# Kernel tuning notes

Measured on AMD Instinct MI355X. Metric: run time of the kernel, lower is better.

## Reference

```python
import jax, jax.numpy as jnp
import numpy as np

B, L, E, H = 32, 2048, 512, 512


def setup_inputs() -> dict:
    key = jax.random.key(0)
    k1, k2, k3, k4 = jax.random.split(key, 4)
    encodings = jax.random.normal(k1, (B, L, E), dtype=jnp.float32)
    lengths = jax.random.randint(k2, (B,), 1, L + 1, dtype=jnp.int32)
    # Glorot-ish scaled params
    W_h = jax.random.normal(k3, (E, H), dtype=jnp.float32) / np.sqrt(E)
    b_h = jnp.zeros((H,), dtype=jnp.float32)
    W_c = jax.random.normal(k4, (H, E), dtype=jnp.float32) / np.sqrt(H)
    return {"encodings": encodings, "lengths": lengths, "W_h": W_h, "b_h": b_h, "W_c": W_c}


def reference(encodings, lengths, W_h, b_h, W_c):
    # encodings: [B, L, E] padded ragged pack; lengths: [B] valid lengths
    mask = jnp.arange(encodings.shape[1])[None, :] < lengths[:, None]  # [B, L]
    # hidden_layer with tanh nonlinearity (TimeDistributedLinear)
    h = jnp.tanh(jnp.einsum('ble,eh->blh', encodings, W_h) + b_h)  # [B, L, H]
    # context_vector (no bias) -> per-feature attention logits [B, L, E]
    att = jnp.einsum('blh,he->ble', h, W_c)
    # timedistributed_softmax: softmax over time axis per sample, per feature
    att = jnp.where(mask[:, :, None], att, -jnp.inf)
    att = jax.nn.softmax(att, axis=1)  # padded positions get weight 0
    # weighted sum over time -> [B, E], then unsqueeze(1)
    out = jnp.sum(att * encodings, axis=1)[:, None, :]  # [B, 1, E]
    return out
```

## Files before the change

### kernel.cpp

```cpp
#include <hip/hip_runtime.h>
#include <math.h>

#define BB 32
#define LL 2048
#define EE 512
#define HH 512
#define WSL 32

typedef __bf16 bf16_t;
typedef bf16_t bf16x8 __attribute__((ext_vector_type(8)));
typedef float f32x4 __attribute__((ext_vector_type(4)));
typedef unsigned short u16x8 __attribute__((ext_vector_type(8)));

__device__ __forceinline__ unsigned short f2bf(float f) {
  unsigned int u = __builtin_bit_cast(unsigned int, f);
  unsigned int r = (u + 0x7FFFu + ((u >> 16) & 1u)) >> 16;
  return (unsigned short)r;
}
__device__ __forceinline__ float bf2f(unsigned short s) {
  unsigned int u = ((unsigned int)s) << 16;
  return __builtin_bit_cast(float, u);
}
__device__ __forceinline__ bf16x8 ld_frag(const unsigned short* p) {
  u16x8 raw = *(const u16x8*)p;
  return __builtin_bit_cast(bf16x8, raw);
}
__device__ __forceinline__ float tanh_fast(float x) {
  x = fminf(fmaxf(x, -15.f), 15.f);
  float e2 = __expf(2.f * x);
  return (e2 - 1.f) / (e2 + 1.f);
}

__device__ __forceinline__ void w_issue(const unsigned short* __restrict__ Wt,
                                        int rbase, int k0, int lane, u16x8 t[4]) {
  const unsigned short* g = Wt + (size_t)(rbase + (lane >> 2)) * 512 + k0 + (lane & 3) * 8;
#pragma unroll
  for (int i = 0; i < 4; i++) t[i] = *(const u16x8*)(g + i * 16 * 512);
}
__device__ __forceinline__ void w_write(unsigned short* buf, int lane, const u16x8 t[4]) {
  unsigned short* d = buf + (lane >> 2) * WSL + (lane & 3) * 8;
#pragma unroll
  for (int i = 0; i < 4; i++) *(u16x8*)(d + i * 16 * WSL) = t[i];
}

__global__ __launch_bounds__(256) void prep_w(
    const float* __restrict__ Wh, const float* __restrict__ Wc,
    unsigned short* __restrict__ WhT, unsigned short* __restrict__ WcT,
    int* __restrict__ q)
{
  if (blockIdx.x == 0 && blockIdx.y == 0 && threadIdx.x == 0) *q = 0;
  const float* src = blockIdx.y ? Wc : Wh;
  unsigned short* dst = blockIdx.y ? WcT : WhT;
  const int tr = (blockIdx.x >> 3) * 64;
  const int tc = (blockIdx.x & 7) * 64;
  const int tid = threadIdx.x;
  __shared__ float tile[64][65];
  for (int i = tid; i < 64 * 16; i += 256) {
    const int r = i >> 4, c4 = (i & 15) << 2;
    const float4 v = *(const float4*)(src + (size_t)(tr + r) * 512 + tc + c4);
    tile[r][c4 + 0] = v.x; tile[r][c4 + 1] = v.y;
    tile[r][c4 + 2] = v.z; tile[r][c4 + 3] = v.w;
  }
  __syncthreads();
  for (int i = tid; i < 64 * 16; i += 256) {
    const int r = i >> 4, c4 = (i & 15) << 2;
    ushort4 pk;
    pk.x = f2bf(tile[c4 + 0][r]); pk.y = f2bf(tile[c4 + 1][r]);
    pk.z = f2bf(tile[c4 + 2][r]); pk.w = f2bf(tile[c4 + 3][r]);
    *(ushort4*)(dst + (size_t)(tc + r) * 512 + tr + c4) = pk;
  }
}

__global__ __launch_bounds__(512, 2) void attn_main(
    const float* __restrict__ enc, const int* __restrict__ lens,
    const unsigned short* __restrict__ WhT, const float* __restrict__ bh,
    const unsigned short* __restrict__ WcT,
    float* __restrict__ pm, float* __restrict__ ps, float* __restrict__ po,
    int* __restrict__ q, int C, int Lc)
{
  const int tid  = threadIdx.x;
  const int wave = tid >> 6;
  const int lane = tid & 63;
  const int quad = lane >> 4;
  const int l15  = lane & 15;
  const int wbase = wave * 64;

  __shared__ __align__(16) unsigned short ebuf[2][32 * 520];
  __shared__ __align__(16) unsigned short wslabS[8 * 2 * 64 * WSL];
  __shared__ __align__(16) float bhS[512];
  __shared__ int itemS;

  unsigned short* sl0 = &wslabS[(wave * 2 + 0) * 64 * WSL];
  unsigned short* sl1 = &wslabS[(wave * 2 + 1) * 64 * WSL];

  bhS[tid] = bh[tid];
  const int nitems = 32 * C;

  if (tid == 0) {
    int it;
    for (;;) {
      it = atomicAdd(q, 1);
      if (it >= nitems || lens[it & 31] > (it >> 5) * Lc) break;
    }
    itemS = it;
  }
  __syncthreads();
  int item = itemS;
  int p = 0;

  float4 eR[8];
  if (item < nitems) {
    const float* src = enc + ((size_t)(item & 31) * LL + (size_t)(item >> 5) * Lc) * EE;
#pragma unroll
    for (int k = 0; k < 8; k++) {
      const int i = tid + k * 512;
      eR[k] = *(const float4*)(src + (size_t)(i >> 7) * EE + ((i & 127) << 2));
    }
  }

#pragma unroll 1
  for (;;) {
    if (item >= nitems) break;
    const int b = item & 31;
    const int c = item >> 5;
    const int l0 = c * Lc;
    const int nvalid = min(lens[b] - l0, Lc);
    const int phase = (item + wave) & 15;
    unsigned short* encA = ebuf[p];
    unsigned short* hS   = ebuf[p ^ 1];

    float stM[4], stS[4], stO[4];
#pragma unroll
    for (int et = 0; et < 4; et++) { stM[et] = -1e30f; stS[et] = 0.f; stO[et] = 0.f; }

    int nextItem = nitems;

#pragma unroll 1
    for (int r0 = 0; r0 < nvalid; r0 += 32) {
      const bool lastPass = (r0 + 32 >= nvalid);

      if (r0 == 0) {
#pragma unroll
        for (int k = 0; k < 8; k++) {
          const int i = tid + k * 512;
          const float4 v = eR[k];
          ushort4 pk;
          pk.x = f2bf(v.x); pk.y = f2bf(v.y); pk.z = f2bf(v.z); pk.w = f2bf(v.w);
          *(ushort4*)&encA[(i >> 7) * 520 + ((i & 127) << 2)] = pk;
        }
      } else {
        const float* encRow = enc + ((size_t)b * LL + l0 + r0) * EE;
        for (int i = tid; i < 32 * 128; i += 512) {
          const int m = i >> 7, e4 = (i & 127) << 2;
          const float4 v = *(const float4*)(encRow + (size_t)m * EE + e4);
          ushort4 pk;
          pk.x = f2bf(v.x); pk.y = f2bf(v.y); pk.z = f2bf(v.z); pk.w = f2bf(v.w);
          *(ushort4*)&encA[m * 520 + e4] = pk;
        }
      }
      if (lastPass && tid == 0) {
        int it;
        for (;;) {
          it = atomicAdd(q, 1);
          if (it >= nitems || lens[it & 31] > (it >> 5) * Lc) break;
        }
        itemS = it;
      }
      __syncthreads();

      f32x4 acc1[4][2];
#pragma unroll
      for (int t = 0; t < 4; t++)
        for (int mt = 0; mt < 2; mt++) acc1[t][mt] = (f32x4){0.f, 0.f, 0.f, 0.f};
      {
        u16x8 tA[4], tB[4];
        w_issue(WhT, wbase, ((0 + phase) & 15) * 32, lane, tA);
        w_issue(WhT, wbase, ((1 + phase) & 15) * 32, lane, tB);
        w_write(sl0, lane, tA);
#pragma unroll 1
        for (int kk = 0; kk < 16; kk += 2) {
          w_write(sl1, lane, tB);
          if (kk + 2 < 16) w_issue(WhT, wbase, ((kk + 2 + phase) & 15) * 32, lane, tA);
          {
            const int k0 = ((kk + phase) & 15) * 32;
            const bf16x8 b0 = ld_frag(&encA[l15 * 520 + k0 + quad * 8]);
            const bf16x8 b1 = ld_frag(&encA[(16 + l15) * 520 + k0 + quad * 8]);
#pragma unroll
            for (int t = 0; t < 4; t++) {
              const bf16x8 af = ld_frag(&sl0[(t * 16 + l15) * WSL + quad * 8]);
              acc1[t][0] = __builtin_amdgcn_mfma_f32_16x16x32_bf16(af, b0, acc1[t][0], 0, 0, 0);
              acc1[t][1] = __builtin_amdgcn_mfma_f32_16x16x32_bf16(af, b1, acc1[t][1], 0, 0, 0);
            }
          }
          if (kk + 2 < 16) w_write(sl0, lane, tA);
          if (kk + 3 < 16) w_issue(WhT, wbase, ((kk + 3 + phase) & 15) * 32, lane, tB);
          {
            const int k0 = ((kk + 1 + phase) & 15) * 32;
            const bf16x8 b0 = ld_frag(&encA[l15 * 520 + k0 + quad * 8]);
            const bf16x8 b1 = ld_frag(&encA[(16 + l15) * 520 + k0 + quad * 8]);
#pragma unroll
            for (int t = 0; t < 4; t++) {
              const bf16x8 af = ld_frag(&sl1[(t * 16 + l15) * WSL + quad * 8]);
              acc1[t][0] = __builtin_amdgcn_mfma_f32_16x16x32_bf16(af, b0, acc1[t][0], 0, 0, 0);
              acc1[t][1] = __builtin_amdgcn_mfma_f32_16x16x32_bf16(af, b1, acc1[t][1], 0, 0, 0);
            }
          }
        }
      }

#pragma unroll
      for (int t = 0; t < 4; t++) {
        const f32x4 bv = *(const f32x4*)&bhS[wbase + t * 16 + quad * 4];
#pragma unroll
        for (int mt = 0; mt < 2; mt++) {
          ushort4 pk;
          pk.x = f2bf(tanh_fast(acc1[t][mt][0] + bv[0]));
          pk.y = f2bf(tanh_fast(acc1[t][mt][1] + bv[1]));
          pk.z = f2bf(tanh_fast(acc1[t][mt][2] + bv[2]));
          pk.w = f2bf(tanh_fast(acc1[t][mt][3] + bv[3]));
          *(ushort4*)&hS[(mt * 16 + l15) * 520 + wbase + t * 16 + quad * 4] = pk;
        }
      }
      __syncthreads();

      f32x4 acc2[2][4];
#pragma unroll
      for (int mt = 0; mt < 2; mt++)
        for (int et = 0; et < 4; et++) acc2[mt][et] = (f32x4){0.f, 0.f, 0.f, 0.f};
      {
        u16x8 tA[4], tB[4];
        w_issue(WcT, wbase, ((0 + phase) & 15) * 32, lane, tA);
        w_issue(WcT, wbase, ((1 + phase) & 15) * 32, lane, tB);
        w_write(sl0, lane, tA);
#pragma unroll 1
        for (int kk = 0; kk < 16; kk += 2) {
          w_write(sl1, lane, tB);
          if (kk + 2 < 16) w_issue(WcT, wbase, ((kk + 2 + phase) & 15) * 32, lane, tA);
          {
            const int k0 = ((kk + phase) & 15) * 32;
            const bf16x8 a0 = ld_frag(&hS[l15 * 520 + k0 + quad * 8]);
            const bf16x8 a1 = ld_frag(&hS[(16 + l15) * 520 + k0 + quad * 8]);
#pragma unroll
            for (int et = 0; et < 4; et++) {
              const bf16x8 bf = ld_frag(&sl0[(et * 16 + l15) * WSL + quad * 8]);
              acc2[0][et] = __builtin_amdgcn_mfma_f32_16x16x32_bf16(a0, bf, acc2[0][et], 0, 0, 0);
              acc2[1][et] = __builtin_amdgcn_mfma_f32_16x16x32_bf16(a1, bf, acc2[1][et], 0, 0, 0);
            }
          }
          if (kk + 2 < 16) w_write(sl0, lane, tA);
          if (kk + 3 < 16) w_issue(WcT, wbase, ((kk + 3 + phase) & 15) * 32, lane, tB);
          {
            const int k0 = ((kk + 1 + phase) & 15) * 32;
            const bf16x8 a0 = ld_frag(&hS[l15 * 520 + k0 + quad * 8]);
            const bf16x8 a1 = ld_frag(&hS[(16 + l15) * 520 + k0 + quad * 8]);
#pragma unroll
            for (int et = 0; et < 4; et++) {
              const bf16x8 bf = ld_frag(&sl1[(et * 16 + l15) * WSL + quad * 8]);
              acc2[0][et] = __builtin_amdgcn_mfma_f32_16x16x32_bf16(a0, bf, acc2[0][et], 0, 0, 0);
              acc2[1][et] = __builtin_amdgcn_mfma_f32_16x16x32_bf16(a1, bf, acc2[1][et], 0, 0, 0);
            }
          }
        }
      }

      if (lastPass) {
        nextItem = itemS;
        if (nextItem < nitems) {
          const float* src = enc + ((size_t)(nextItem & 31) * LL + (size_t)(nextItem >> 5) * Lc) * EE;
#pragma unroll
          for (int k = 0; k < 8; k++) {
            const int i = tid + k * 512;
            eR[k] = *(const float4*)(src + (size_t)(i >> 7) * EE + ((i & 127) << 2));
          }
        }
      }

      bool ok[2][4];
#pragma unroll
      for (int mt = 0; mt < 2; mt++)
#pragma unroll
        for (int r = 0; r < 4; r++)
          ok[mt][r] = (r0 + mt * 16 + quad * 4 + r) < nvalid;

#pragma unroll
      for (int et = 0; et < 4; et++) {
        const int e = wbase + et * 16 + l15;
        float v[2][4];
        float lm = -1e30f;
#pragma unroll
        for (int mt = 0; mt < 2; mt++)
#pragma unroll
          for (int r = 0; r < 4; r++) {
            v[mt][r] = ok[mt][r] ? acc2[mt][et][r] : -1e30f;
            lm = fmaxf(lm, v[mt][r]);
          }
        lm = fmaxf(lm, __shfl_xor(lm, 16));
        lm = fmaxf(lm, __shfl_xor(lm, 32));
        float ls = 0.f, lo = 0.f;
#pragma unroll
        for (int mt = 0; mt < 2; mt++)
#pragma unroll
          for (int r = 0; r < 4; r++) {
            const float pexp = __expf(v[mt][r] - lm);
            const float ev = bf2f(encA[(mt * 16 + quad * 4 + r) * 520 + e]);
            ls += pexp;
            lo += pexp * ev;
          }
        ls += __shfl_xor(ls, 16); ls += __shfl_xor(ls, 32);
        lo += __shfl_xor(lo, 16); lo += __shfl_xor(lo, 32);
        const float Mn = fmaxf(stM[et], lm);
        const float sc = __expf(stM[et] - Mn);
        const float st = __expf(lm - Mn);
        stS[et] = stS[et] * sc + ls * st;
        stO[et] = stO[et] * sc + lo * st;
        stM[et] = Mn;
      }
      __syncthreads();
    }

    if (quad == 0) {
      const size_t base = ((size_t)b * C + c) * EE;
#pragma unroll
      for (int et = 0; et < 4; et++) {
        const int e = wbase + et * 16 + l15;
        pm[base + e] = stM[et];
        ps[base + e] = stS[et];
        po[base + e] = stO[et];
      }
    }

    item = nextItem;
    p ^= 1;
  }
}

__global__ __launch_bounds__(256) void attn_combine(
    const float* __restrict__ pm, const float* __restrict__ ps,
    const float* __restrict__ po, const int* __restrict__ lens,
    float* __restrict__ out, int C, int Lc)
{
  const int b  = blockIdx.y;
  const int e  = blockIdx.x * 64 + (threadIdx.x & 63);
  const int g  = threadIdx.x >> 6;
  const int n  = lens[b];
  const int cmax = min(C, (n + Lc - 1) / Lc);

  float M = -1e30f, S = 0.f, O = 0.f;
  for (int c = g; c < cmax; c += 4) {
    const size_t base = ((size_t)b * C + c) * EE;
    const float m = pm[base + e];
    const float s = ps[base + e];
    const float o = po[base + e];
    const float Mn  = fmaxf(M, m);
    const float sc0 = __expf(M - Mn);
    const float sc1 = __expf(m - Mn);
    S = S * sc0 + s * sc1;
    O = O * sc0 + o * sc1;
    M = Mn;
  }

  __shared__ float sM[4][64], sS[4][64], sO[4][64];
  sM[g][threadIdx.x & 63] = M;
  sS[g][threadIdx.x & 63] = S;
  sO[g][threadIdx.x & 63] = O;
  __syncthreads();

  if (g == 0) {
    const int le = threadIdx.x & 63;
    float Mt = sM[0][le], St = sS[0][le], Ot = sO[0][le];
#pragma unroll
    for (int gg = 1; gg < 4; gg++) {
      const float m = sM[gg][le];
      const float Mn  = fmaxf(Mt, m);
      const float sc0 = __expf(Mt - Mn);
      const float sc1 = __expf(m - Mn);
      St = St * sc0 + sS[gg][le] * sc1;
      Ot = Ot * sc0 + sO[gg][le] * sc1;
      Mt = Mn;
    }
    out[(size_t)b * EE + e] = Ot / St;
  }
}

extern "C" void kernel_launch(void* const* d_in, const int* in_sizes, int n_in,
                              void* d_out, int out_size, void* d_ws, size_t ws_size,
                              hipStream_t stream) {
  const float* enc  = (const float*)d_in[0];
  const int*   lens = (const int*)d_in[1];
  const float* Wh   = (const float*)d_in[2];
  const float* bh   = (const float*)d_in[3];
  const float* Wc   = (const float*)d_in[4];
  float* out = (float*)d_out;

  const size_t wbytes = (size_t)512 * 512 * sizeof(unsigned short);
  int C = 64;
  while (C > 8 && ws_size < (size_t)3 * BB * C * EE * sizeof(float) + 2 * wbytes + 64)
    C >>= 1;
  const int Lc = LL / C;

  float* pm = (float*)d_ws;
  float* ps = pm + (size_t)BB * C * EE;
  float* po = ps + (size_t)BB * C * EE;
  unsigned short* WhT = (unsigned short*)(po + (size_t)BB * C * EE);
  unsigned short* WcT = WhT + (size_t)512 * 512;
  int* q = (int*)(WcT + (size_t)512 * 512);

  prep_w<<<dim3(64, 2), 256, 0, stream>>>(Wh, Wc, WhT, WcT, q);
  attn_main<<<dim3(256), 512, 0, stream>>>(enc, lens, WhT, bh, WcT, pm, ps, po, q, C, Lc);
  attn_combine<<<dim3(8, BB), 256, 0, stream>>>(pm, ps, po, lens, out, C, Lc);
}
```

Before: 276.7 us.

## Load weight MFMA fragments directly from global into registers, drop LDS slab

Weight fragments for both GEMMs are now loaded straight from global/L2 into registers in MFMA layout, double-buffered across k-steps, instead of being staged through a per-wave LDS slab. This removes LDS writes and reads for the weights and frees 32KB of shared memory per block, which is meant to allow more resident blocks per CU, so the grid is doubled to 512 persistent blocks. In exchange each fragment load is a 16-byte strided global access per lane, relying on L2 hits, and register pressure rises.

Measured after the change: 343.5 us. 1.24x slower.

```diff
diff --git a/kernel.cpp b/kernel.cpp
--- a/kernel.cpp
+++ b/kernel.cpp
@@ -5,7 +5,6 @@
 #define LL 2048
 #define EE 512
 #define HH 512
-#define WSL 32
 
 typedef __bf16 bf16_t;
 typedef bf16_t bf16x8 __attribute__((ext_vector_type(8)));
@@ -31,16 +30,10 @@
   return (e2 - 1.f) / (e2 + 1.f);
 }
 
-__device__ __forceinline__ void w_issue(const unsigned short* __restrict__ Wt,
-                                        int rbase, int k0, int lane, u16x8 t[4]) {
-  const unsigned short* g = Wt + (size_t)(rbase + (lane >> 2)) * 512 + k0 + (lane & 3) * 8;
-#pragma unroll
-  for (int i = 0; i < 4; i++) t[i] = *(const u16x8*)(g + i * 16 * 512);
-}
-__device__ __forceinline__ void w_write(unsigned short* buf, int lane, const u16x8 t[4]) {
-  unsigned short* d = buf + (lane >> 2) * WSL + (lane & 3) * 8;
-#pragma unroll
-  for (int i = 0; i < 4; i++) *(u16x8*)(d + i * 16 * WSL) = t[i];
+__device__ __forceinline__ void frag_issue(const unsigned short* __restrict__ g,
+                                           int k0, bf16x8 f[4]) {
+#pragma unroll
+  for (int i = 0; i < 4; i++) f[i] = ld_frag(g + (size_t)i * 16 * 512 + k0);
 }
 
 __global__ __launch_bounds__(256) void prep_w(
@@ -86,12 +79,8 @@
   const int wbase = wave * 64;
 
   __shared__ __align__(16) unsigned short ebuf[2][32 * 520];
-  __shared__ __align__(16) unsigned short wslabS[8 * 2 * 64 * WSL];
   __shared__ __align__(16) float bhS[512];
   __shared__ int itemS;
-
-  unsigned short* sl0 = &wslabS[(wave * 2 + 0) * 64 * WSL];
-  unsigned short* sl1 = &wslabS[(wave * 2 + 1) * 64 * WSL];
 
   bhS[tid] = bh[tid];
   const int nitems = 32 * C;
@@ -173,37 +162,33 @@
       for (int t = 0; t < 4; t++)
         for (int mt = 0; mt < 2; mt++) acc1[t][mt] = (f32x4){0.f, 0.f, 0.f, 0.f};
       {
-        u16x8 tA[4], tB[4];
-        w_issue(WhT, wbase, ((0 + phase) & 15) * 32, lane, tA);
-        w_issue(WhT, wbase, ((1 + phase) & 15) * 32, lane, tB);
-        w_write(sl0, lane, tA);
+        const unsigned short* baseW = WhT + (size_t)(wbase + l15) * 512 + quad * 8;
+        bf16x8 fA[4], fB[4];
+        frag_issue(baseW, ((0 + phase) & 15) * 32, fA);
+        frag_issue(baseW, ((1 + phase) & 15) * 32, fB);
 #pragma unroll 1
         for (int kk = 0; kk < 16; kk += 2) {
-          w_write(sl1, lane, tB);
-          if (kk + 2 < 16) w_issue(WhT, wbase, ((kk + 2 + phase) & 15) * 32, lane, tA);
           {
             const int k0 = ((kk + phase) & 15) * 32;
             const bf16x8 b0 = ld_frag(&encA[l15 * 520 + k0 + quad * 8]);
             const bf16x8 b1 = ld_frag(&encA[(16 + l15) * 520 + k0 + quad * 8]);
 #pragma unroll
             for (int t = 0; t < 4; t++) {
-              const bf16x8 af = ld_frag(&sl0[(t * 16 + l15) * WSL + quad * 8]);
-              acc1[t][0] = __builtin_amdgcn_mfma_f32_16x16x32_bf16(af, b0, acc1[t][0], 0, 0, 0);
-              acc1[t][1] = __builtin_amdgcn_mfma_f32_16x16x32_bf16(af, b1, acc1[t][1], 0, 0, 0);
+              acc1[t][0] = __builtin_amdgcn_mfma_f32_16x16x32_bf16(fA[t], b0, acc1[t][0], 0, 0, 0);
+              acc1[t][1] = __builtin_amdgcn_mfma_f32_16x16x32_bf16(fA[t], b1, acc1[t][1], 0, 0, 0);
             }
-          }
-          if (kk + 2 < 16) w_write(sl0, lane, tA);
-          if (kk + 3 < 16) w_issue(WhT, wbase, ((kk + 3 + phase) & 15) * 32, lane, tB);
+            if (kk + 2 < 16) frag_issue(baseW, ((kk + 2 + phase) & 15) * 32, fA);
+          }
           {
             const int k0 = ((kk + 1 + phase) & 15) * 32;
             const bf16x8 b0 = ld_frag(&encA[l15 * 520 + k0 + quad * 8]);
             const bf16x8 b1 = ld_frag(&encA[(16 + l15) * 520 + k0 + quad * 8]);
 #pragma unroll
             for (int t = 0; t < 4; t++) {
-              const bf16x8 af = ld_frag(&sl1[(t * 16 + l15) * WSL + quad * 8]);
-              acc1[t][0] = __builtin_amdgcn_mfma_f32_16x16x32_bf16(af, b0, acc1[t][0], 0, 0, 0);
-              acc1[t][1] = __builtin_amdgcn_mfma_f32_16x16x32_bf16(af, b1, acc1[t][1], 0, 0, 0);
+              acc1[t][0] = __builtin_amdgcn_mfma_f32_16x16x32_bf16(fB[t], b0, acc1[t][0], 0, 0, 0);
+              acc1[t][1] = __builtin_amdgcn_mfma_f32_16x16x32_bf16(fB[t], b1, acc1[t][1], 0, 0, 0);
             }
+            if (kk + 3 < 16) frag_issue(baseW, ((kk + 3 + phase) & 15) * 32, fB);
           }
         }
       }
@@ -228,37 +213,33 @@
       for (int mt = 0; mt < 2; mt++)
         for (int et = 0; et < 4; et++) acc2[mt][et] = (f32x4){0.f, 0.f, 0.f, 0.f};
       {
-        u16x8 tA[4], tB[4];
-        w_issue(WcT, wbase, ((0 + phase) & 15) * 32, lane, tA);
-        w_issue(WcT, wbase, ((1 + phase) & 15) * 32, lane, tB);
-        w_write(sl0, lane, tA);
+        const unsigned short* baseW = WcT + (size_t)(wbase + l15) * 512 + quad * 8;
+        bf16x8 fA[4], fB[4];
+        frag_issue(baseW, ((0 + phase) & 15) * 32, fA);
+        frag_issue(baseW, ((1 + phase) & 15) * 32, fB);
 #pragma unroll 1
         for (int kk = 0; kk < 16; kk += 2) {
-          w_write(sl1, lane, tB);
-          if (kk + 2 < 16) w_issue(WcT, wbase, ((kk + 2 + phase) & 15) * 32, lane, tA);
           {
             const int k0 = ((kk + phase) & 15) * 32;
             const bf16x8 a0 = ld_frag(&hS[l15 * 520 + k0 + quad * 8]);
             const bf16x8 a1 = ld_frag(&hS[(16 + l15) * 520 + k0 + quad * 8]);
 #pragma unroll
             for (int et = 0; et < 4; et++) {
-              const bf16x8 bf = ld_frag(&sl0[(et * 16 + l15) * WSL + quad * 8]);
-              acc2[0][et] = __builtin_amdgcn_mfma_f32_16x16x32_bf16(a0, bf, acc2[0][et], 0, 0, 0);
-              acc2[1][et] = __builtin_amdgcn_mfma_f32_16x16x32_bf16(a1, bf, acc2[1][et], 0, 0, 0);
+              acc2[0][et] = __builtin_amdgcn_mfma_f32_16x16x32_bf16(a0, fA[et], acc2[0][et], 0, 0, 0);
+              acc2[1][et] = __builtin_amdgcn_mfma_f32_16x16x32_bf16(a1, fA[et], acc2[1][et], 0, 0, 0);
             }
-          }
-          if (kk + 2 < 16) w_write(sl0, lane, tA);
-          if (kk + 3 < 16) w_issue(WcT, wbase, ((kk + 3 + phase) & 15) * 32, lane, tB);
+            if (kk + 2 < 16) frag_issue(baseW, ((kk + 2 + phase) & 15) * 32, fA);
+          }
           {
             const int k0 = ((kk + 1 + phase) & 15) * 32;
             const bf16x8 a0 = ld_frag(&hS[l15 * 520 + k0 + quad * 8]);
             const bf16x8 a1 = ld_frag(&hS[(16 + l15) * 520 + k0 + quad * 8]);
 #pragma unroll
             for (int et = 0; et < 4; et++) {
-              const bf16x8 bf = ld_frag(&sl1[(et * 16 + l15) * WSL + quad * 8]);
-              acc2[0][et] = __builtin_amdgcn_mfma_f32_16x16x32_bf16(a0, bf, acc2[0][et], 0, 0, 0);
-              acc2[1][et] = __builtin_amdgcn_mfma_f32_16x16x32_bf16(a1, bf, acc2[1][et], 0, 0, 0);
+              acc2[0][et] = __builtin_amdgcn_mfma_f32_16x16x32_bf16(a0, fB[et], acc2[0][et], 0, 0, 0);
+              acc2[1][et] = __builtin_amdgcn_mfma_f32_16x16x32_bf16(a1, fB[et], acc2[1][et], 0, 0, 0);
             }
+            if (kk + 3 < 16) frag_issue(baseW, ((kk + 3 + phase) & 15) * 32, fB);
           }
         }
       }
@@ -406,6 +387,6 @@
   int* q = (int*)(WcT + (size_t)512 * 512);
 
   prep_w<<<dim3(64, 2), 256, 0, stream>>>(Wh, Wc, WhT, WcT, q);
-  attn_main<<<dim3(256), 512, 0, stream>>>(enc, lens, WhT, bh, WcT, pm, ps, po, q, C, Lc);
+  attn_main<<<dim3(512), 512, 0, stream>>>(enc, lens, WhT, bh, WcT, pm, ps, po, q, C, Lc);
   attn_combine<<<dim3(8, BB), 256, 0, stream>>>(pm, ps, po, lens, out, C, Lc);
 }
```
